# Performance work log

Hardware: AMD Instinct MI355X
Metric: run time of the kernel (lower is better)

The kernel has to match this reference:

```python
import jax, jax.numpy as jnp
import numpy as np

EMBED_DIM = 1024
NUM_HEADS = 16
HEAD_DIM = EMBED_DIM // NUM_HEADS
T = 1024
B = 4
NEG = -100000.0


def apply_rope(x):
    # x: [batch, heads, seq, head_dim]; split-half rotation (non-interleaved)
    seq_len, head_dim = x.shape[2], x.shape[3]
    half = head_dim // 2
    theta = 1.0 / (10000.0 ** (jnp.arange(half, dtype=jnp.float32) / half))
    pos = jnp.arange(seq_len, dtype=jnp.float32)
    sinusoid = pos[:, None] * theta[None, :]          # [seq, half]
    sin = jnp.sin(sinusoid)[None, None]
    cos = jnp.cos(sinusoid)[None, None]
    x1, x2 = x[..., :half], x[..., half:]
    return jnp.concatenate([x1 * cos - x2 * sin, x1 * sin + x2 * cos], axis=-1)


def setup_inputs() -> dict:
    key = jax.random.key(0)
    ks = jax.random.split(key, 9)
    scale = EMBED_DIM ** -0.5
    return {
        "query": jax.random.normal(ks[0], (T, B, EMBED_DIM), jnp.float32),
        "key": jax.random.normal(ks[1], (T, B, EMBED_DIM), jnp.float32),
        "value": jax.random.normal(ks[2], (T, B, EMBED_DIM), jnp.float32),
        "key_padding_mask": jax.random.randint(ks[3], (B, T), 0, 2) > 0,
        "attn_mask": jax.random.randint(ks[4], (B, T, T), 0, 2) > 0,
        "q_w": jax.random.normal(ks[5], (EMBED_DIM, EMBED_DIM), jnp.float32) * scale,
        "k_w": jax.random.normal(ks[6], (EMBED_DIM, EMBED_DIM), jnp.float32) * scale,
        "v_w": jax.random.normal(ks[7], (EMBED_DIM, EMBED_DIM), jnp.float32) * scale,
        "o_w": jax.random.normal(ks[8], (EMBED_DIM, EMBED_DIM), jnp.float32) * scale,
    }


def reference(query, key, value, key_padding_mask, attn_mask, q_w, k_w, v_w, o_w):
    Tq, batch, _ = query.shape
    Tk = key.shape[0]
    # projections (torch Linear: y = x @ W.T), weights are [out, in]
    def split_heads(x):  # [t, b, D] -> [b, h, t, d]
        return x.reshape(x.shape[0], batch, NUM_HEADS, HEAD_DIM).transpose(1, 2, 0, 3)
    Q = split_heads(query @ q_w.T)
    K = split_heads(key @ k_w.T)
    V = split_heads(value @ v_w.T)
    Q = apply_rope(Q)
    K = apply_rope(K)
    # additive mask: (attn_mask + key_padding_mask) * -1e5, broadcast over heads
    mask = attn_mask.astype(jnp.float32)[:, None]                     # [b,1,Tq,Tk]
    mask = mask + key_padding_mask.astype(jnp.float32)[:, None, None, :]
    mask = mask * NEG
    scores = jnp.einsum('bhqd,bhkd->bhqk', Q, K) * (HEAD_DIM ** -0.5) + mask
    attn = jax.nn.softmax(scores, axis=-1)
    out = jnp.einsum('bhqk,bhkd->bhqd', attn, V)                      # [b,h,Tq,d]
    out = out.transpose(2, 0, 1, 3).reshape(Tq, batch, EMBED_DIM)
    return out @ o_w.T
```

## Files before the change

kernel.cpp:

```cpp
#include <hip/hip_runtime.h>
#include <hip/hip_bf16.h>
#include <math.h>

typedef __bf16 bf16x8 __attribute__((ext_vector_type(8)));
typedef float f32x4 __attribute__((ext_vector_type(4)));
typedef unsigned short u16x8 __attribute__((ext_vector_type(8)));
typedef unsigned short u16x4 __attribute__((ext_vector_type(4)));


#define OFF_XQ   0u
#define OFF_XK   4194304u
#define OFF_XV   8388608u
#define OFF_WQ   12582912u
#define OFF_WK   13631488u
#define OFF_WV   14680064u
#define OFF_WO   15728640u
#define OFF_QR   16777216u
#define OFF_KR   20971520u
#define OFF_VROW 25165824u
#define OFF_VT   29360128u
#define OFF_AO   33554432u
#define OFF_MW   37748736u

static __device__ __forceinline__ unsigned short f2bf(float f){
  unsigned u = __builtin_bit_cast(unsigned, f);
  u += 0x7FFFu + ((u >> 16) & 1u);
  return (unsigned short)(u >> 16);
}

static __device__ __forceinline__ f32x4 mfma16(bf16x8 a, bf16x8 b, f32x4 c){
  return __builtin_amdgcn_mfma_f32_16x16x32_bf16(a, b, c, 0, 0, 0);
}

static __device__ __forceinline__ void glds16(const unsigned short* g, unsigned short* l){
  __builtin_amdgcn_global_load_lds(
      (const __attribute__((address_space(1))) unsigned int*)g,
      (__attribute__((address_space(3))) unsigned int*)l, 16, 0, 0);
}

__global__ __launch_bounds__(256) void cvt_all(
    const float* __restrict__ q, const float* __restrict__ k, const float* __restrict__ v,
    const float* __restrict__ qw, const float* __restrict__ kw, const float* __restrict__ vw,
    const float* __restrict__ ow, unsigned short* __restrict__ ws)
{
  size_t e = ((size_t)blockIdx.x * 256 + threadIdx.x) * 4;
  const float* s;
  if      (e < 4194304u)  { s = q  + e; }
  else if (e < 8388608u)  { s = k  + (e - 4194304u); }
  else if (e < 12582912u) { s = v  + (e - 8388608u); }
  else if (e < 13631488u) { s = qw + (e - 12582912u); }
  else if (e < 14680064u) { s = kw + (e - 13631488u); }
  else if (e < 15728640u) { s = vw + (e - 14680064u); }
  else                    { s = ow + (e - 15728640u); }
  float4 f = *(const float4*)s;
  u16x4 o;
  o[0] = f2bf(f.x); o[1] = f2bf(f.y); o[2] = f2bf(f.z); o[3] = f2bf(f.w);
  *(u16x4*)(ws + e) = o;
}

__global__ __launch_bounds__(256) void pack_mask(
    const int* __restrict__ am, const int* __restrict__ kpm, unsigned long long* __restrict__ mw)
{
  int idx = blockIdx.x * 256 + threadIdx.x;
  int w = idx & 15, q = (idx >> 4) & 1023, b = idx >> 14;
  const int* ap = am + ((size_t)(b*1024 + q))*1024 + w*64;
  const int* kp = kpm + b*1024 + w*64;
  unsigned long long bits = 0ull;
#pragma unroll
  for (int j = 0; j < 64; j += 4){
    int4 a = *(const int4*)(ap + j);
    int4 c = *(const int4*)(kp + j);
    unsigned long long m =
        (unsigned long long)(((a.x | c.x) != 0) ? 1 : 0)
      | ((unsigned long long)(((a.y | c.y) != 0) ? 1 : 0) << 1)
      | ((unsigned long long)(((a.z | c.z) != 0) ? 1 : 0) << 2)
      | ((unsigned long long)(((a.w | c.w) != 0) ? 1 : 0) << 3);
    bits |= (m << j);
  }
  mw[idx] = bits;
}

static __device__ __forceinline__ void gemm_core(
    const unsigned short* __restrict__ Ap, const unsigned short* __restrict__ Wp,
    unsigned short (*As)[4096], unsigned short (*Bs)[4096],
    int tid, int wr, int wc, int l16, int lg, f32x4 (&acc)[4][4])
{
  const int su = (lg ^ (l16 & 3) ^ (l16 >> 2)) & 3;

  glds16(Ap,         &As[0][(size_t)tid*8]);
  glds16(Ap + 65536, &As[0][2048 + (size_t)tid*8]);
  glds16(Wp,         &Bs[0][(size_t)tid*8]);
  glds16(Wp + 65536, &Bs[0][2048 + (size_t)tid*8]);

  for (int kt = 0; kt < 32; ++kt){
    const int cur = kt & 1;
    if (kt < 31){
      glds16(Ap + (kt+1)*32,         &As[cur^1][(size_t)tid*8]);
      glds16(Ap + 65536 + (kt+1)*32, &As[cur^1][2048 + (size_t)tid*8]);
      glds16(Wp + (kt+1)*32,         &Bs[cur^1][(size_t)tid*8]);
      glds16(Wp + 65536 + (kt+1)*32, &Bs[cur^1][2048 + (size_t)tid*8]);
      asm volatile("s_waitcnt vmcnt(4)" ::: "memory");
    } else {
      asm volatile("s_waitcnt vmcnt(0)" ::: "memory");
    }
    __builtin_amdgcn_sched_barrier(0);
    __builtin_amdgcn_s_barrier();
    __builtin_amdgcn_sched_barrier(0);
    const unsigned short* Ab = As[cur];
    const unsigned short* Bb = Bs[cur];
    bf16x8 af[4], bfr[4];
#pragma unroll
    for (int mt = 0; mt < 4; ++mt) af[mt]  = *(const bf16x8*)&Ab[(wr*64 + mt*16 + l16)*32 + su*8];
#pragma unroll
    for (int nt = 0; nt < 4; ++nt) bfr[nt] = *(const bf16x8*)&Bb[(wc*64 + nt*16 + l16)*32 + su*8];
#pragma unroll
    for (int mt = 0; mt < 4; ++mt)
#pragma unroll
      for (int nt = 0; nt < 4; ++nt)
        acc[mt][nt] = mfma16(af[mt], bfr[nt], acc[mt][nt]);
    __builtin_amdgcn_sched_barrier(0);
    __builtin_amdgcn_s_barrier();
    __builtin_amdgcn_sched_barrier(0);
  }
}

static __device__ __forceinline__ void tile_map(int bx, int by, int& m0, int& n0){
  const int lin = bx + (by << 3);
  const int xcd = lin & 7, j = lin >> 3;
  m0 = ((xcd << 2) + (j >> 3)) * 128;
  n0 = (j & 7) * 128;
}

__global__ __launch_bounds__(256) void gemm_qkv(unsigned short* __restrict__ ws)
{
  const int tid = threadIdx.x;
  const int lane = tid & 63, wave = tid >> 6;
  const int wr = wave >> 1, wc = wave & 1;
  const int l16 = lane & 15, lg = lane >> 4;
  int m0, n0;
  tile_map(blockIdx.x, blockIdx.y, m0, n0);
  const int z = blockIdx.z;

  const unsigned short* A = ws + OFF_XQ + (unsigned)z * 4194304u;
  const unsigned short* W = ws + OFF_WQ + (unsigned)z * 1048576u;

  __shared__ unsigned short As[2][4096];
  __shared__ unsigned short Bs[2][4096];

  f32x4 acc[4][4];
#pragma unroll
  for (int i = 0; i < 4; ++i)
#pragma unroll
    for (int j = 0; j < 4; ++j)
      acc[i][j] = (f32x4){0.f, 0.f, 0.f, 0.f};

  const int r0 = tid >> 2;
  const int c0 = (((tid & 3) ^ (r0 & 3) ^ ((r0 >> 2) & 3)) << 3);
  gemm_core(A + (size_t)(m0 + r0)*1024 + c0, W + (size_t)(n0 + r0)*1024 + c0,
            As, Bs, tid, wr, wc, l16, lg, acc);

  if (z == 2){
    unsigned short* outB = ws + OFF_VROW;
#pragma unroll
    for (int mt = 0; mt < 4; ++mt)
#pragma unroll
      for (int nt = 0; nt < 4; ++nt)
#pragma unroll
        for (int r = 0; r < 4; ++r){
          int m = m0 + wr*64 + mt*16 + lg*4 + r;
          int n = n0 + wc*64 + nt*16 + l16;
          int t = m >> 2, bi = m & 3, h = n >> 6, d = n & 63;
          outB[(((size_t)(bi*16 + h))*1024 + t)*64 + d] = f2bf(acc[mt][nt][r]);
        }
  } else {
    unsigned short* outB = ws + (z == 0 ? OFF_QR : OFF_KR);
    const float oscale = (z == 0) ? 0.125f : 1.0f;
#pragma unroll
    for (int mt = 0; mt < 4; ++mt){
      int mbase = m0 + wr*64 + mt*16 + lg*4;
      int t = mbase >> 2;
#pragma unroll
      for (int nt = 0; nt < 2; ++nt){
        int n = n0 + wc*64 + nt*16 + l16;
        int h = n >> 6, d = n & 31;
        float theta = expf((float)d * -0.28782313662425575f);
        float ang = (float)t * theta;
        float sv = sinf(ang), cv = cosf(ang);
#pragma unroll
        for (int r = 0; r < 4; ++r){
          float x1 = acc[mt][nt][r]     * oscale;
          float x2 = acc[mt][nt + 2][r] * oscale;
          float o1 = x1*cv - x2*sv;
          float o2 = x1*sv + x2*cv;
          size_t ob = (((size_t)(r*16 + h))*1024 + t)*64;
          outB[ob + d]      = f2bf(o1);
          outB[ob + d + 32] = f2bf(o2);
        }
      }
    }
  }
}

__global__ __launch_bounds__(256) void gemm_o(
    const unsigned short* __restrict__ A, const unsigned short* __restrict__ W,
    float* __restrict__ outF)
{
  const int tid = threadIdx.x;
  const int lane = tid & 63, wave = tid >> 6;
  const int wr = wave >> 1, wc = wave & 1;
  const int l16 = lane & 15, lg = lane >> 4;
  int m0, n0;
  tile_map(blockIdx.x, blockIdx.y, m0, n0);

  __shared__ unsigned short As[2][4096];
  __shared__ unsigned short Bs[2][4096];

  f32x4 acc[4][4];
#pragma unroll
  for (int i = 0; i < 4; ++i)
#pragma unroll
    for (int j = 0; j < 4; ++j)
      acc[i][j] = (f32x4){0.f, 0.f, 0.f, 0.f};

  const int r0 = tid >> 2;
  const int c0 = (((tid & 3) ^ (r0 & 3) ^ ((r0 >> 2) & 3)) << 3);
  gemm_core(A + (size_t)(m0 + r0)*1024 + c0, W + (size_t)(n0 + r0)*1024 + c0,
            As, Bs, tid, wr, wc, l16, lg, acc);

#pragma unroll
  for (int mt = 0; mt < 4; ++mt)
#pragma unroll
    for (int nt = 0; nt < 4; ++nt)
#pragma unroll
      for (int r = 0; r < 4; ++r){
        int m = m0 + wr*64 + mt*16 + lg*4 + r;
        int n = n0 + wc*64 + nt*16 + l16;
        outF[(size_t)m*1024 + n] = acc[mt][nt][r];
      }
}

__global__ __launch_bounds__(256) void vtrans(
    const unsigned short* __restrict__ Vrow, unsigned short* __restrict__ Vt)
{
  const int bh = blockIdx.y;
  const int t0 = blockIdx.x * 64;
  const unsigned short* src = Vrow + (size_t)bh*65536 + (size_t)t0*64;
  unsigned short* dst = Vt + (size_t)bh*65536 + t0;
  __shared__ unsigned short tile[64][65];
  const int tid = threadIdx.x;
#pragma unroll
  for (int i = 0; i < 16; ++i){
    int idx = tid + i*256;
    int r = idx >> 6, c = idx & 63;
    tile[r][c] = src[r*64 + c];
  }
  __syncthreads();
#pragma unroll
  for (int i = 0; i < 16; ++i){
    int idx = tid + i*256;
    int d = idx >> 6, c = idx & 63;
    dst[(size_t)d*1024 + c] = tile[c][d];
  }
}

__global__ __launch_bounds__(512, 4) void attn_kernel(
    const unsigned short* __restrict__ Qr, const unsigned short* __restrict__ Kr,
    const unsigned short* __restrict__ Vt, const unsigned long long* __restrict__ mw,
    unsigned short* __restrict__ AO)
{
  const int tid = threadIdx.x;
  const int lane = tid & 63, w = tid >> 6;
  const int l16 = lane & 15, lg = lane >> 4;
  const int wg = blockIdx.x;
  const int xcd = wg & 7;
  const int bh = xcd * 8 + ((wg >> 3) & 7);
  const int qt = wg >> 6;
  const int b = bh >> 4, h = bh & 15;
  const int q0 = qt * 128 + w * 16;
  const size_t hb = (size_t)bh * 65536;
  const unsigned long long* mwp = mw + (size_t)b * 16384 + (size_t)(q0 + lg*4) * 16;

  __shared__ unsigned short Ks[2][4096];
  __shared__ unsigned short Vs[2][4096];
  __shared__ unsigned short Plds[8][1024];
  unsigned short* Pw = Plds[w];

  const int srow = tid >> 3;
  const int scol = (tid & 7) ^ (srow & 7);
  const unsigned short* Ksrc = Kr + hb + (size_t)srow*64   + scol*8;
  const unsigned short* Vsrc = Vt + hb + (size_t)srow*1024 + scol*8;

  bf16x8 qf0 = *(const bf16x8*)&Qr[hb + (size_t)(q0 + l16)*64 + lg*8];
  bf16x8 qf1 = *(const bf16x8*)&Qr[hb + (size_t)(q0 + l16)*64 + 32 + lg*8];

  f32x4 O[4];
  float ls[4] = {0.f, 0.f, 0.f, 0.f};
#pragma unroll
  for (int nd = 0; nd < 4; ++nd) O[nd] = (f32x4){0.f, 0.f, 0.f, 0.f};

  glds16(Ksrc, &Ks[0][(size_t)tid*8]);
  glds16(Vsrc, &Vs[0][(size_t)tid*8]);

#pragma unroll 1
  for (int kt = 0; kt < 16; ++kt){
    const int cur = kt & 1;
    if (kt < 15){
      glds16(Ksrc + (kt+1)*4096, &Ks[cur^1][(size_t)tid*8]);
      glds16(Vsrc + (kt+1)*64,   &Vs[cur^1][(size_t)tid*8]);
      asm volatile("s_waitcnt vmcnt(2)" ::: "memory");
    } else {
      asm volatile("s_waitcnt vmcnt(0)" ::: "memory");
    }
    __builtin_amdgcn_sched_barrier(0);
    __builtin_amdgcn_s_barrier();
    __builtin_amdgcn_sched_barrier(0);

    const unsigned short* Kb = Ks[cur];
    const unsigned short* Vb = Vs[cur];

    unsigned long long bits[4];
#pragma unroll
    for (int r = 0; r < 4; ++r) bits[r] = mwp[r*16 + kt];

    bf16x8 kf[4][2];
#pragma unroll
    for (int nk = 0; nk < 4; ++nk)
#pragma unroll
      for (int kk = 0; kk < 2; ++kk){
        int row = nk*16 + l16;
        kf[nk][kk] = *(const bf16x8*)&Kb[row*64 + (((kk*4 + lg) ^ (row & 7)) << 3)];
      }

    f32x4 s[4];
    __builtin_amdgcn_s_setprio(1);
#pragma unroll
    for (int nk = 0; nk < 4; ++nk){
      f32x4 t0 = (f32x4){0.f, 0.f, 0.f, 0.f};
      t0 = mfma16(qf0, kf[nk][0], t0);
      t0 = mfma16(qf1, kf[nk][1], t0);
      s[nk] = t0;
    }
    __builtin_amdgcn_s_setprio(0);

    bf16x8 vf[4][2];
#pragma unroll
    for (int nd = 0; nd < 4; ++nd)
#pragma unroll
      for (int kk = 0; kk < 2; ++kk){
        int row = nd*16 + l16;
        vf[nd][kk] = *(const bf16x8*)&Vb[row*64 + (((kk*4 + lg) ^ (row & 7)) << 3)];
      }

    float p[4][4];
#pragma unroll
    for (int nk = 0; nk < 4; ++nk)
#pragma unroll
      for (int r = 0; r < 4; ++r){
        float pen = ((bits[r] >> (nk*16 + l16)) & 1ull) ? -100000.0f : 0.0f;
        p[nk][r] = __expf(s[nk][r] + pen);
      }
#pragma unroll
    for (int r = 0; r < 4; ++r)
      ls[r] += (p[0][r] + p[1][r]) + (p[2][r] + p[3][r]);

#pragma unroll
    for (int nk = 0; nk < 4; ++nk)
#pragma unroll
      for (int r = 0; r < 4; ++r){
        int row = lg*4 + r;
        int col = (nk*16 + l16) ^ ((row & 7) << 3);
        Pw[row*64 + col] = f2bf(p[nk][r]);
      }
    asm volatile("s_waitcnt lgkmcnt(0)" ::: "memory");
    __builtin_amdgcn_sched_barrier(0);

    __builtin_amdgcn_s_setprio(1);
#pragma unroll
    for (int kk = 0; kk < 2; ++kk){
      int row = l16;
      int colg = (kk*32 + lg*8) ^ ((row & 7) << 3);
      bf16x8 pf = *(const bf16x8*)&Pw[row*64 + colg];
#pragma unroll
      for (int nd = 0; nd < 4; ++nd)
        O[nd] = mfma16(pf, vf[nd][kk], O[nd]);
    }
    __builtin_amdgcn_s_setprio(0);

    __builtin_amdgcn_sched_barrier(0);
    __builtin_amdgcn_s_barrier();
    __builtin_amdgcn_sched_barrier(0);
  }

#pragma unroll
  for (int r = 0; r < 4; ++r){
    float v = ls[r];
#pragma unroll
    for (int off = 1; off < 16; off <<= 1) v += __shfl_xor(v, off, 64);
    float inv = 1.0f / v;
    int q = q0 + lg*4 + r;
    size_t rowb = ((size_t)q*4 + b)*1024 + h*64;
#pragma unroll
    for (int nd = 0; nd < 4; ++nd)
      AO[rowb + nd*16 + l16] = f2bf(O[nd][r] * inv);
  }
}

extern "C" void kernel_launch(void* const* d_in, const int* in_sizes, int n_in,
                              void* d_out, int out_size, void* d_ws, size_t ws_size,
                              hipStream_t stream)
{
  const float* q   = (const float*)d_in[0];
  const float* k   = (const float*)d_in[1];
  const float* v   = (const float*)d_in[2];
  const int*   kpm = (const int*)d_in[3];
  const int*   am  = (const int*)d_in[4];
  const float* qw  = (const float*)d_in[5];
  const float* kw  = (const float*)d_in[6];
  const float* vw  = (const float*)d_in[7];
  const float* ow  = (const float*)d_in[8];
  unsigned short* ws = (unsigned short*)d_ws;
  unsigned long long* mw = (unsigned long long*)(ws + OFF_MW);

  cvt_all<<<16384, 256, 0, stream>>>(q, k, v, qw, kw, vw, ow, ws);
  pack_mask<<<256, 256, 0, stream>>>(am, kpm, mw);

  gemm_qkv<<<dim3(8, 32, 3), 256, 0, stream>>>(ws);
  vtrans<<<dim3(16, 64), 256, 0, stream>>>(ws + OFF_VROW, ws + OFF_VT);
  attn_kernel<<<512, 512, 0, stream>>>(ws + OFF_QR, ws + OFF_KR, ws + OFF_VT,
                                       mw, ws + OFF_AO);
  gemm_o<<<dim3(8, 32), 256, 0, stream>>>(ws + OFF_AO, ws + OFF_WO, (float*)d_out);
}
```

Measured before the change: 126.6 us.

## Triple-buffer GEMM LDS pipeline, fold log2e into Q scale, use exp2 and native bf16 cast

The shared GEMM core moves from double to triple buffering of LDS tiles. Loads for step kt+2 are issued right after the barrier, which removes the second barrier per k-step. The Q projection scale now includes log2(e), so the attention softmax can call exp2 directly instead of __expf. Manual bf16 rounding is replaced with the compiler's native __bf16 conversion in the attention kernel. These changes raise LDS use per GEMM block, which may lower occupancy, and the penalty is now applied in the exp2 domain. That penalty is unscaled, but it still drives masked entries to zero.

Measured after the change: 149.8 us. 18.3% more time.

```diff
diff --git a/kernel.cpp b/kernel.cpp
--- a/kernel.cpp
+++ b/kernel.cpp
@@ -28,6 +28,10 @@
   return (unsigned short)(u >> 16);
 }
 
+static __device__ __forceinline__ unsigned short bfcast(float f){
+  return __builtin_bit_cast(unsigned short, (__bf16)f);
+}
+
 static __device__ __forceinline__ f32x4 mfma16(bf16x8 a, bf16x8 b, f32x4 c){
   return __builtin_amdgcn_mfma_f32_16x16x32_bf16(a, b, c, 0, 0, 0);
 }
@@ -87,25 +91,23 @@
 {
   const int su = (lg ^ (l16 & 3) ^ (l16 >> 2)) & 3;
 
-  glds16(Ap,         &As[0][(size_t)tid*8]);
-  glds16(Ap + 65536, &As[0][2048 + (size_t)tid*8]);
-  glds16(Wp,         &Bs[0][(size_t)tid*8]);
-  glds16(Wp + 65536, &Bs[0][2048 + (size_t)tid*8]);
-
+#define STG1(buf, kt) do{ \
+    glds16(Ap + (kt)*32,         &As[buf][(size_t)tid*8]); \
+    glds16(Ap + 65536 + (kt)*32, &As[buf][2048 + (size_t)tid*8]); \
+    glds16(Wp + (kt)*32,         &Bs[buf][(size_t)tid*8]); \
+    glds16(Wp + 65536 + (kt)*32, &Bs[buf][2048 + (size_t)tid*8]); }while(0)
+
+  STG1(0, 0);
+  STG1(1, 1);
+
+  int cur = 0, sb = 2;
   for (int kt = 0; kt < 32; ++kt){
-    const int cur = kt & 1;
-    if (kt < 31){
-      glds16(Ap + (kt+1)*32,         &As[cur^1][(size_t)tid*8]);
-      glds16(Ap + 65536 + (kt+1)*32, &As[cur^1][2048 + (size_t)tid*8]);
-      glds16(Wp + (kt+1)*32,         &Bs[cur^1][(size_t)tid*8]);
-      glds16(Wp + 65536 + (kt+1)*32, &Bs[cur^1][2048 + (size_t)tid*8]);
-      asm volatile("s_waitcnt vmcnt(4)" ::: "memory");
-    } else {
-      asm volatile("s_waitcnt vmcnt(0)" ::: "memory");
-    }
+    if (kt < 31) asm volatile("s_waitcnt vmcnt(4)" ::: "memory");
+    else         asm volatile("s_waitcnt vmcnt(0)" ::: "memory");
     __builtin_amdgcn_sched_barrier(0);
     __builtin_amdgcn_s_barrier();
     __builtin_amdgcn_sched_barrier(0);
+    if (kt < 30) STG1(sb, kt + 2);
     const unsigned short* Ab = As[cur];
     const unsigned short* Bb = Bs[cur];
     bf16x8 af[4], bfr[4];
@@ -118,10 +120,10 @@
 #pragma unroll
       for (int nt = 0; nt < 4; ++nt)
         acc[mt][nt] = mfma16(af[mt], bfr[nt], acc[mt][nt]);
-    __builtin_amdgcn_sched_barrier(0);
-    __builtin_amdgcn_s_barrier();
-    __builtin_amdgcn_sched_barrier(0);
-  }
+    cur = (cur == 2) ? 0 : cur + 1;
+    sb  = (sb  == 2) ? 0 : sb  + 1;
+  }
+#undef STG1
 }
 
 static __device__ __forceinline__ void tile_map(int bx, int by, int& m0, int& n0){
@@ -144,8 +146,8 @@
   const unsigned short* A = ws + OFF_XQ + (unsigned)z * 4194304u;
   const unsigned short* W = ws + OFF_WQ + (unsigned)z * 1048576u;
 
-  __shared__ unsigned short As[2][4096];
-  __shared__ unsigned short Bs[2][4096];
+  __shared__ unsigned short As[3][4096];
+  __shared__ unsigned short Bs[3][4096];
 
   f32x4 acc[4][4];
 #pragma unroll
@@ -174,7 +176,7 @@
         }
   } else {
     unsigned short* outB = ws + (z == 0 ? OFF_QR : OFF_KR);
-    const float oscale = (z == 0) ? 0.125f : 1.0f;
+    const float oscale = (z == 0) ? 0.18033688011118886f : 1.0f;
 #pragma unroll
     for (int mt = 0; mt < 4; ++mt){
       int mbase = m0 + wr*64 + mt*16 + lg*4;
@@ -212,8 +214,8 @@
   int m0, n0;
   tile_map(blockIdx.x, blockIdx.y, m0, n0);
 
-  __shared__ unsigned short As[2][4096];
-  __shared__ unsigned short Bs[2][4096];
+  __shared__ unsigned short As[3][4096];
+  __shared__ unsigned short Bs[3][4096];
 
   f32x4 acc[4][4];
 #pragma unroll
@@ -357,7 +359,7 @@
 #pragma unroll
       for (int r = 0; r < 4; ++r){
         float pen = ((bits[r] >> (nk*16 + l16)) & 1ull) ? -100000.0f : 0.0f;
-        p[nk][r] = __expf(s[nk][r] + pen);
+        p[nk][r] = __builtin_exp2f(s[nk][r] + pen);
       }
 #pragma unroll
     for (int r = 0; r < 4; ++r)
@@ -369,7 +371,7 @@
       for (int r = 0; r < 4; ++r){
         int row = lg*4 + r;
         int col = (nk*16 + l16) ^ ((row & 7) << 3);
-        Pw[row*64 + col] = f2bf(p[nk][r]);
+        Pw[row*64 + col] = bfcast(p[nk][r]);
       }
     asm volatile("s_waitcnt lgkmcnt(0)" ::: "memory");
     __builtin_amdgcn_sched_barrier(0);
@@ -401,7 +403,7 @@
     size_t rowb = ((size_t)q*4 + b)*1024 + h*64;
 #pragma unroll
     for (int nd = 0; nd < 4; ++nd)
-      AO[rowb + nd*16 + l16] = f2bf(O[nd][r] * inv);
+      AO[rowb + nd*16 + l16] = bfcast(O[nd][r] * inv);
   }
 }
 
```
